# Kernel tuning notes

Measured on AMD Instinct MI355X. Metric: run time of the kernel, lower is better.

The kernel has to match this reference:

```python
import jax, jax.numpy as jnp
import numpy as np


def setup_inputs() -> dict:
    key = jax.random.key(0)
    k1, k2, k3, k4 = jax.random.split(key, 4)
    N, C_in, C_out, H, W, K = 32, 128, 256, 56, 56, 3
    x = jax.random.normal(k1, (N, C_in, H, W), dtype=jnp.float32)
    # ternary weights in {-1, 0, +1}, stored as int8 like the torch buffer
    w_q = jax.random.randint(k2, (C_out, C_in, K, K), -1, 2).astype(jnp.int8)
    s = jax.random.uniform(k3, (C_out, 1, 1), dtype=jnp.float32) + 0.5
    bias = jax.random.normal(k4, (C_out,), dtype=jnp.float32)
    return {"x": x, "w_q": w_q, "s": s, "bias": bias}


def reference(x, w_q, s, bias):
    # y = conv2d(x, w_q.float()) * s + bias, stride=1, padding=1, dilation=1, groups=1
    w = w_q.astype(x.dtype)  # ternary {-1,0,+1} cast to float, as in torch
    y = jax.lax.conv_general_dilated(
        x, w,
        window_strides=(1, 1),
        padding=((1, 1), (1, 1)),
        lhs_dilation=(1, 1),
        rhs_dilation=(1, 1),
        dimension_numbers=("NCHW", "OIHW", "NCHW"),
        feature_group_count=1,
    )
    y = y * s  # s: [C_out,1,1] broadcasts over [N,C_out,H,W]
    y = y + bias.reshape(1, -1, 1, 1)
    return y
```

## Files before the change

kernel.cpp:

```cpp
#include <hip/hip_runtime.h>
#include <hip/hip_bf16.h>

typedef unsigned short ushort_t;

#define N_IMG 32
#define C_IN  128
#define C_OUT 256
#define H_SZ  56
#define W_SZ  56
#define HW_SZ (H_SZ * W_SZ)
#define K_TOT (C_IN * 9)
#define SP_TOT (N_IMG * HW_SZ)

typedef __attribute__((ext_vector_type(8))) short bf16x8;
typedef __attribute__((ext_vector_type(4))) float floatx4;

__device__ __forceinline__ void gl_lds16(const ushort_t* g, ushort_t* l) {
  __builtin_amdgcn_global_load_lds(
      (const __attribute__((address_space(1))) void*)g,
      (__attribute__((address_space(3))) void*)l, 16, 0, 0);
}

__device__ __forceinline__ ushort_t f2bf(float f) {
  __hip_bfloat16 b = __float2bfloat16(f);
  return *reinterpret_cast<ushort_t*>(&b);
}

__global__ void wtrans_kernel(const int* __restrict__ wq, ushort_t* __restrict__ wt,
                              ushort_t* __restrict__ zeros) {
  int tid = threadIdx.x;
  if (blockIdx.x == 0 && tid < 128) zeros[tid] = 0;
  int idx = blockIdx.x * 256 + tid;
  if (idx >= C_OUT * K_TOT) return;
  int co = idx / K_TOT;
  int k  = idx - co * K_TOT;
  int tap = k >> 7;
  int c   = k & 127;
  int kh = tap / 3, kw = tap - kh * 3;
  int v = wq[((co * C_IN + c) * 3 + kh) * 3 + kw];
  wt[idx] = f2bf((float)v);
}

__global__ void xtrans_kernel(const float* __restrict__ x, ushort_t* __restrict__ xt) {
  __shared__ float tile[C_IN * W_SZ];
  int b = blockIdx.x;
  int n = b / H_SZ, h = b - n * H_SZ;
  int tid = threadIdx.x;
  const float* xbase = x + (size_t)n * C_IN * HW_SZ + h * W_SZ;
  for (int idx = tid; idx < C_IN * W_SZ; idx += 256) {
    int c = idx / W_SZ, w = idx - c * W_SZ;
    tile[idx] = xbase[(size_t)c * HW_SZ + w];
  }
  __syncthreads();
  ushort_t* obase = xt + (size_t)b * W_SZ * C_IN;
  for (int idx = tid; idx < W_SZ * (C_IN / 2); idx += 256) {
    int w  = idx >> 6;
    int ci = (idx & 63) * 2;
    unsigned int p = (unsigned int)f2bf(tile[ci * W_SZ + w]) |
                     ((unsigned int)f2bf(tile[(ci + 1) * W_SZ + w]) << 16);
    *(unsigned int*)&obase[(size_t)w * C_IN + ci] = p;
  }
}

__global__ __launch_bounds__(256) void bitconv_kernel(
    const ushort_t* __restrict__ wt, const ushort_t* __restrict__ xt,
    const ushort_t* __restrict__ zeros,
    const float* __restrict__ s, const float* __restrict__ bias,
    float* __restrict__ out) {
  __shared__ ushort_t As[128 * 32];
  __shared__ ushort_t Bs[128 * 32];

  int bid = blockIdx.x;
  int co0 = (bid & 1) * 128;
  int sp0 = (bid >> 1) * 128;

  int tid  = threadIdx.x;
  int lane = tid & 63;
  int wid  = tid >> 6;
  int l15  = lane & 15;
  int quad = lane >> 4;
  int lrow = lane >> 2;
  int lk8  = (lane & 3) * 8;
  int wave_m = (wid >> 1) * 64;
  int wave_n = (wid & 1) * 64;

  const ushort_t* a_src[2];
  ushort_t* a_dst[2];
#pragma unroll
  for (int i = 0; i < 2; ++i) {
    int arow = wid * 32 + i * 16 + lrow;
    a_src[i] = wt + (size_t)(co0 + arow) * K_TOT + lk8;
    a_dst[i] = &As[(wid * 32 + i * 16) * 32];
  }

  int bh[2], bw[2];
  const ushort_t* b_img[2];
  ushort_t* b_dst[2];
#pragma unroll
  for (int i = 0; i < 2; ++i) {
    int sp   = sp0 + wid * 32 + i * 16 + lrow;
    int nimg = sp / HW_SZ;
    int rem  = sp - nimg * HW_SZ;
    bh[i] = rem / W_SZ;
    bw[i] = rem - bh[i] * W_SZ;
    b_img[i] = xt + (size_t)nimg * HW_SZ * C_IN;
    b_dst[i] = &Bs[(wid * 32 + i * 16) * 32];
  }

  floatx4 acc[4][4];
#pragma unroll
  for (int mi = 0; mi < 4; ++mi)
#pragma unroll
    for (int ni = 0; ni < 4; ++ni)
      acc[mi][ni] = (floatx4){0.f, 0.f, 0.f, 0.f};

  for (int tap = 0; tap < 9; ++tap) {
    int dh = tap / 3 - 1;
    int dw = tap - (dh + 1) * 3 - 1;
    const ushort_t* bsrc[2];
#pragma unroll
    for (int i = 0; i < 2; ++i) {
      int hh2 = bh[i] + dh, ww2 = bw[i] + dw;
      bool valid = (hh2 >= 0) & (hh2 < H_SZ) & (ww2 >= 0) & (ww2 < W_SZ);
      bsrc[i] = valid ? (b_img[i] + (size_t)(hh2 * W_SZ + ww2) * C_IN + lk8)
                      : (zeros + lk8);
    }
    int ktap = tap * C_IN;
#pragma unroll
    for (int c0 = 0; c0 < C_IN; c0 += 32) {
#pragma unroll
      for (int i = 0; i < 2; ++i) {
        gl_lds16(a_src[i] + ktap + c0, a_dst[i]);
        gl_lds16(bsrc[i] + c0, b_dst[i]);
      }
      __syncthreads();
      bf16x8 af[4], bfv[4];
#pragma unroll
      for (int mi = 0; mi < 4; ++mi)
        af[mi] = *(const bf16x8*)&As[(wave_m + mi * 16 + l15) * 32 + quad * 8];
#pragma unroll
      for (int ni = 0; ni < 4; ++ni)
        bfv[ni] = *(const bf16x8*)&Bs[(wave_n + ni * 16 + l15) * 32 + quad * 8];
#pragma unroll
      for (int mi = 0; mi < 4; ++mi)
#pragma unroll
        for (int ni = 0; ni < 4; ++ni)
          acc[mi][ni] = __builtin_amdgcn_mfma_f32_16x16x32_bf16(
              af[mi], bfv[ni], acc[mi][ni], 0, 0, 0);
      __syncthreads();
    }
  }

  int spl_[4], nimg_[4];
#pragma unroll
  for (int ni = 0; ni < 4; ++ni) {
    int sp = sp0 + wave_n + ni * 16 + l15;
    int nimg = sp / HW_SZ;
    nimg_[ni] = nimg;
    spl_[ni]  = sp - nimg * HW_SZ;
  }
#pragma unroll
  for (int mi = 0; mi < 4; ++mi) {
#pragma unroll
    for (int r = 0; r < 4; ++r) {
      int co = co0 + wave_m + mi * 16 + quad * 4 + r;
      float sv = s[co];
      float bv = bias[co];
#pragma unroll
      for (int ni = 0; ni < 4; ++ni) {
        out[((size_t)nimg_[ni] * C_OUT + co) * HW_SZ + spl_[ni]] =
            acc[mi][ni][r] * sv + bv;
      }
    }
  }
}

extern "C" void kernel_launch(void* const* d_in, const int* in_sizes, int n_in,
                              void* d_out, int out_size, void* d_ws, size_t ws_size,
                              hipStream_t stream) {
  const float* x    = (const float*)d_in[0];
  const int*   wq   = (const int*)d_in[1];
  const float* s    = (const float*)d_in[2];
  const float* bias = (const float*)d_in[3];
  float* out = (float*)d_out;

  char* ws = (char*)d_ws;
  ushort_t* zeros = (ushort_t*)ws;
  ushort_t* wt    = (ushort_t*)(ws + 256);
  ushort_t* xt    = (ushort_t*)(ws + 590080);

  hipLaunchKernelGGL(wtrans_kernel, dim3((C_OUT * K_TOT) / 256), dim3(256), 0, stream,
                     wq, wt, zeros);
  hipLaunchKernelGGL(xtrans_kernel, dim3(N_IMG * H_SZ), dim3(256), 0, stream, x, xt);
  hipLaunchKernelGGL(bitconv_kernel, dim3((C_OUT / 128) * (SP_TOT / 128)), dim3(256),
                     0, stream, wt, xt, zeros, s, bias, out);
}
```

Measured before the change: 250.5 us.

## Double K-tile depth, swizzle block order, and retile input transpose kernel

The conv GEMM main loop now stages 64 channels per LDS tile instead of 32 and issues two MFMA k-substeps per barrier pair. This halves the number of __syncthreads rounds, at the cost of doubling LDS use. Block indices are remapped so that pairs of co-tiles for nearby spatial tiles run adjacently, which is meant to improve L2 reuse of the input. The NCHW-to-NHWC bf16 transpose kernel now uses 64x64 tiles with float4 loads and a padded LDS stride, to cut bank conflicts and improve coalescing.

```diff
diff --git a/kernel.cpp b/kernel.cpp
--- a/kernel.cpp
+++ b/kernel.cpp
@@ -41,24 +41,37 @@
   wt[idx] = f2bf((float)v);
 }
 
-__global__ void xtrans_kernel(const float* __restrict__ x, ushort_t* __restrict__ xt) {
-  __shared__ float tile[C_IN * W_SZ];
+#define LDT 69
+__global__ __launch_bounds__(256) void xtrans_kernel(const float* __restrict__ x,
+                                                     ushort_t* __restrict__ xt) {
+  __shared__ float tile[64 * LDT];
   int b = blockIdx.x;
-  int n = b / H_SZ, h = b - n * H_SZ;
-  int tid = threadIdx.x;
-  const float* xbase = x + (size_t)n * C_IN * HW_SZ + h * W_SZ;
-  for (int idx = tid; idx < C_IN * W_SZ; idx += 256) {
-    int c = idx / W_SZ, w = idx - c * W_SZ;
-    tile[idx] = xbase[(size_t)c * HW_SZ + w];
+  int n = b / 98;
+  int r = b - n * 98;
+  int cg = r / 49;
+  int hwg = r - cg * 49;
+  int hw0 = hwg * 64, c0 = cg * 64;
+  int t = threadIdx.x;
+  int cl = t >> 4;
+  int f4 = t & 15;
+  const float* xb = x + ((size_t)(n * C_IN + c0) * HW_SZ + hw0);
+#pragma unroll
+  for (int p = 0; p < 4; ++p) {
+    int c = p * 16 + cl;
+    float4 v = *(const float4*)(xb + (size_t)c * HW_SZ + f4 * 4);
+    float* dst = &tile[c * LDT + f4 * 4];
+    dst[0] = v.x; dst[1] = v.y; dst[2] = v.z; dst[3] = v.w;
   }
   __syncthreads();
-  ushort_t* obase = xt + (size_t)b * W_SZ * C_IN;
-  for (int idx = tid; idx < W_SZ * (C_IN / 2); idx += 256) {
-    int w  = idx >> 6;
-    int ci = (idx & 63) * 2;
-    unsigned int p = (unsigned int)f2bf(tile[ci * W_SZ + w]) |
-                     ((unsigned int)f2bf(tile[(ci + 1) * W_SZ + w]) << 16);
-    *(unsigned int*)&obase[(size_t)w * C_IN + ci] = p;
+  int cp  = t & 31;
+  int hwl = t >> 5;
+  ushort_t* ob = xt + (size_t)(n * HW_SZ + hw0) * C_IN + c0;
+#pragma unroll
+  for (int p = 0; p < 8; ++p) {
+    int hw = p * 8 + hwl;
+    unsigned int u = (unsigned int)f2bf(tile[(2 * cp) * LDT + hw]) |
+                     ((unsigned int)f2bf(tile[(2 * cp + 1) * LDT + hw]) << 16);
+    *(unsigned int*)&ob[(size_t)hw * C_IN + 2 * cp] = u;
   }
 }
 
@@ -67,44 +80,35 @@
     const ushort_t* __restrict__ zeros,
     const float* __restrict__ s, const float* __restrict__ bias,
     float* __restrict__ out) {
-  __shared__ ushort_t As[128 * 32];
-  __shared__ ushort_t Bs[128 * 32];
-
-  int bid = blockIdx.x;
-  int co0 = (bid & 1) * 128;
-  int sp0 = (bid >> 1) * 128;
+  __shared__ ushort_t As[128 * 64];
+  __shared__ ushort_t Bs[128 * 64];
+
+  int d = blockIdx.x;
+  int sp_idx = (d >> 4) * 8 + (d & 7);
+  int co0 = ((d >> 3) & 1) * 128;
+  int sp0 = sp_idx * 128;
 
   int tid  = threadIdx.x;
   int lane = tid & 63;
   int wid  = tid >> 6;
   int l15  = lane & 15;
   int quad = lane >> 4;
-  int lrow = lane >> 2;
-  int lk8  = (lane & 3) * 8;
+  int lrow8 = lane >> 3;
+  int lk8   = (lane & 7) * 8;
   int wave_m = (wid >> 1) * 64;
   int wave_n = (wid & 1) * 64;
 
-  const ushort_t* a_src[2];
-  ushort_t* a_dst[2];
-#pragma unroll
-  for (int i = 0; i < 2; ++i) {
-    int arow = wid * 32 + i * 16 + lrow;
-    a_src[i] = wt + (size_t)(co0 + arow) * K_TOT + lk8;
-    a_dst[i] = &As[(wid * 32 + i * 16) * 32];
-  }
-
-  int bh[2], bw[2];
-  const ushort_t* b_img[2];
-  ushort_t* b_dst[2];
-#pragma unroll
-  for (int i = 0; i < 2; ++i) {
-    int sp   = sp0 + wid * 32 + i * 16 + lrow;
+  const ushort_t* a_src0 = wt + (size_t)(co0 + wid * 32 + lrow8) * K_TOT + lk8;
+  int bh[4], bw[4];
+  const ushort_t* b_img[4];
+#pragma unroll
+  for (int j = 0; j < 4; ++j) {
+    int sp   = sp0 + wid * 32 + j * 8 + lrow8;
     int nimg = sp / HW_SZ;
     int rem  = sp - nimg * HW_SZ;
-    bh[i] = rem / W_SZ;
-    bw[i] = rem - bh[i] * W_SZ;
-    b_img[i] = xt + (size_t)nimg * HW_SZ * C_IN;
-    b_dst[i] = &Bs[(wid * 32 + i * 16) * 32];
+    bh[j] = rem / W_SZ;
+    bw[j] = rem - bh[j] * W_SZ;
+    b_img[j] = xt + (size_t)nimg * HW_SZ * C_IN;
   }
 
   floatx4 acc[4][4];
@@ -117,36 +121,42 @@
   for (int tap = 0; tap < 9; ++tap) {
     int dh = tap / 3 - 1;
     int dw = tap - (dh + 1) * 3 - 1;
-    const ushort_t* bsrc[2];
-#pragma unroll
-    for (int i = 0; i < 2; ++i) {
-      int hh2 = bh[i] + dh, ww2 = bw[i] + dw;
+    const ushort_t* bsrc[4];
+#pragma unroll
+    for (int j = 0; j < 4; ++j) {
+      int hh2 = bh[j] + dh, ww2 = bw[j] + dw;
       bool valid = (hh2 >= 0) & (hh2 < H_SZ) & (ww2 >= 0) & (ww2 < W_SZ);
-      bsrc[i] = valid ? (b_img[i] + (size_t)(hh2 * W_SZ + ww2) * C_IN + lk8)
+      bsrc[j] = valid ? (b_img[j] + (size_t)(hh2 * W_SZ + ww2) * C_IN + lk8)
                       : (zeros + lk8);
     }
     int ktap = tap * C_IN;
 #pragma unroll
-    for (int c0 = 0; c0 < C_IN; c0 += 32) {
-#pragma unroll
-      for (int i = 0; i < 2; ++i) {
-        gl_lds16(a_src[i] + ktap + c0, a_dst[i]);
-        gl_lds16(bsrc[i] + c0, b_dst[i]);
+    for (int c0 = 0; c0 < C_IN; c0 += 64) {
+#pragma unroll
+      for (int j = 0; j < 4; ++j) {
+        gl_lds16(a_src0 + (size_t)j * 8 * K_TOT + ktap + c0,
+                 &As[(wid * 32 + j * 8) * 64]);
+        gl_lds16(bsrc[j] + c0, &Bs[(wid * 32 + j * 8) * 64]);
       }
       __syncthreads();
-      bf16x8 af[4], bfv[4];
-#pragma unroll
-      for (int mi = 0; mi < 4; ++mi)
-        af[mi] = *(const bf16x8*)&As[(wave_m + mi * 16 + l15) * 32 + quad * 8];
-#pragma unroll
-      for (int ni = 0; ni < 4; ++ni)
-        bfv[ni] = *(const bf16x8*)&Bs[(wave_n + ni * 16 + l15) * 32 + quad * 8];
-#pragma unroll
-      for (int mi = 0; mi < 4; ++mi)
+#pragma unroll
+      for (int ksub = 0; ksub < 2; ++ksub) {
+        bf16x8 af[4], bfv[4];
+#pragma unroll
+        for (int mi = 0; mi < 4; ++mi)
+          af[mi] = *(const bf16x8*)&As[(wave_m + mi * 16 + l15) * 64 +
+                                       ksub * 32 + quad * 8];
 #pragma unroll
         for (int ni = 0; ni < 4; ++ni)
-          acc[mi][ni] = __builtin_amdgcn_mfma_f32_16x16x32_bf16(
-              af[mi], bfv[ni], acc[mi][ni], 0, 0, 0);
+          bfv[ni] = *(const bf16x8*)&Bs[(wave_n + ni * 16 + l15) * 64 +
+                                        ksub * 32 + quad * 8];
+#pragma unroll
+        for (int mi = 0; mi < 4; ++mi)
+#pragma unroll
+          for (int ni = 0; ni < 4; ++ni)
+            acc[mi][ni] = __builtin_amdgcn_mfma_f32_16x16x32_bf16(
+                af[mi], bfv[ni], acc[mi][ni], 0, 0, 0);
+      }
       __syncthreads();
     }
   }
@@ -191,7 +201,7 @@
 
   hipLaunchKernelGGL(wtrans_kernel, dim3((C_OUT * K_TOT) / 256), dim3(256), 0, stream,
                      wq, wt, zeros);
-  hipLaunchKernelGGL(xtrans_kernel, dim3(N_IMG * H_SZ), dim3(256), 0, stream, x, xt);
+  hipLaunchKernelGGL(xtrans_kernel, dim3(N_IMG * 98), dim3(256), 0, stream, x, xt);
   hipLaunchKernelGGL(bitconv_kernel, dim3((C_OUT / 128) * (SP_TOT / 128)), dim3(256),
                      0, stream, wt, xt, zeros, s, bias, out);
 }
```

New measurement: 239.8 us. -4.3%, faster.

## Pre-pad input to 64-wide rows and tile spatial dimension by image rows

Applied to the files above, without the earlier changes.

Input is transposed into a zero-padded NHWC bf16 buffer with 58 rows of 64 columns, so the conv GEMM loads each tap by a fixed offset with no boundary checks or zero-buffer redirect. Spatial tiles become two padded image rows, with a masked store of the 56 valid columns, and blocks are remapped so consecutive tiles land on the same XCD. This removes per-tap address math and branches but spends about an eighth of the MFMA work on padding columns and writes a larger intermediate.

```diff
diff --git a/kernel.cpp b/kernel.cpp
--- a/kernel.cpp
+++ b/kernel.cpp
@@ -10,7 +10,9 @@
 #define W_SZ  56
 #define HW_SZ (H_SZ * W_SZ)
 #define K_TOT (C_IN * 9)
-#define SP_TOT (N_IMG * HW_SZ)
+#define WP 64
+#define HP 58
+#define ROW_E (WP * C_IN)
 
 typedef __attribute__((ext_vector_type(8))) short bf16x8;
 typedef __attribute__((ext_vector_type(4))) float floatx4;
@@ -26,11 +28,8 @@
   return *reinterpret_cast<ushort_t*>(&b);
 }
 
-__global__ void wtrans_kernel(const int* __restrict__ wq, ushort_t* __restrict__ wt,
-                              ushort_t* __restrict__ zeros) {
-  int tid = threadIdx.x;
-  if (blockIdx.x == 0 && tid < 128) zeros[tid] = 0;
-  int idx = blockIdx.x * 256 + tid;
+__global__ void wtrans_kernel(const int* __restrict__ wq, ushort_t* __restrict__ wt) {
+  int idx = blockIdx.x * 256 + threadIdx.x;
   if (idx >= C_OUT * K_TOT) return;
   int co = idx / K_TOT;
   int k  = idx - co * K_TOT;
@@ -41,70 +40,85 @@
   wt[idx] = f2bf((float)v);
 }
 
-__global__ void xtrans_kernel(const float* __restrict__ x, ushort_t* __restrict__ xt) {
-  __shared__ float tile[C_IN * W_SZ];
+__global__ __launch_bounds__(256) void xpad_kernel(const float* __restrict__ x,
+                                                   ushort_t* __restrict__ xp) {
   int b = blockIdx.x;
-  int n = b / H_SZ, h = b - n * H_SZ;
-  int tid = threadIdx.x;
-  const float* xbase = x + (size_t)n * C_IN * HW_SZ + h * W_SZ;
-  for (int idx = tid; idx < C_IN * W_SZ; idx += 256) {
-    int c = idx / W_SZ, w = idx - c * W_SZ;
-    tile[idx] = xbase[(size_t)c * HW_SZ + w];
+  int t = threadIdx.x;
+  ushort_t* row = xp + (size_t)b * ROW_E;
+  int n = b / HP;
+  int h1 = b - n * HP;
+  if (b >= N_IMG * HP || h1 == 0 || h1 == HP - 1) {
+    uint4 z = {0u, 0u, 0u, 0u};
+    uint4* r4 = (uint4*)row;
+#pragma unroll
+    for (int i = 0; i < 4; ++i) r4[i * 256 + t] = z;
+    return;
+  }
+  __shared__ float tile[C_IN * 57];
+  int h = h1 - 1;
+  const float* xb = x + (size_t)n * C_IN * HW_SZ + h * W_SZ;
+#pragma unroll
+  for (int i = 0; i < 7; ++i) {
+    int idx = i * 256 + t;
+    int c = idx / 14, f = idx - c * 14;
+    float4 v = *(const float4*)(xb + (size_t)c * HW_SZ + f * 4);
+    float* dst = &tile[c * 57 + f * 4];
+    dst[0] = v.x; dst[1] = v.y; dst[2] = v.z; dst[3] = v.w;
   }
   __syncthreads();
-  ushort_t* obase = xt + (size_t)b * W_SZ * C_IN;
-  for (int idx = tid; idx < W_SZ * (C_IN / 2); idx += 256) {
-    int w  = idx >> 6;
-    int ci = (idx & 63) * 2;
-    unsigned int p = (unsigned int)f2bf(tile[ci * W_SZ + w]) |
-                     ((unsigned int)f2bf(tile[(ci + 1) * W_SZ + w]) << 16);
-    *(unsigned int*)&obase[(size_t)w * C_IN + ci] = p;
+  unsigned int* r32 = (unsigned int*)row;
+#pragma unroll
+  for (int i = 0; i < 16; ++i) {
+    int idx = i * 256 + t;
+    int wp = idx >> 6, cp = idx & 63;
+    unsigned int u = 0;
+    if (wp >= 1 && wp <= W_SZ) {
+      int w = wp - 1;
+      u = (unsigned int)f2bf(tile[(2 * cp) * 57 + w]) |
+          ((unsigned int)f2bf(tile[(2 * cp + 1) * 57 + w]) << 16);
+    }
+    r32[wp * 64 + cp] = u;
   }
 }
 
 __global__ __launch_bounds__(256) void bitconv_kernel(
-    const ushort_t* __restrict__ wt, const ushort_t* __restrict__ xt,
-    const ushort_t* __restrict__ zeros,
+    const ushort_t* __restrict__ wt, const ushort_t* __restrict__ xp,
     const float* __restrict__ s, const float* __restrict__ bias,
     float* __restrict__ out) {
   __shared__ ushort_t As[128 * 32];
   __shared__ ushort_t Bs[128 * 32];
 
-  int bid = blockIdx.x;
-  int co0 = (bid & 1) * 128;
-  int sp0 = (bid >> 1) * 128;
+  int d = blockIdx.x;
+  int xcd = d & 7;
+  int r   = d >> 3;
+  int co0 = (r & 1) * 128;
+  int sp_tile = xcd * 112 + (r >> 1);
+  int nh0 = sp_tile * 2;
+  int n  = nh0 / H_SZ;
+  int hh = nh0 - n * H_SZ;
 
   int tid  = threadIdx.x;
   int lane = tid & 63;
   int wid  = tid >> 6;
   int l15  = lane & 15;
   int quad = lane >> 4;
-  int lrow = lane >> 2;
-  int lk8  = (lane & 3) * 8;
   int wave_m = (wid >> 1) * 64;
   int wave_n = (wid & 1) * 64;
+  int lrow = lane >> 2;
+  int lchk = (lane & 3) * 8;
 
   const ushort_t* a_src[2];
+  const ushort_t* b_src[2];
   ushort_t* a_dst[2];
-#pragma unroll
-  for (int i = 0; i < 2; ++i) {
-    int arow = wid * 32 + i * 16 + lrow;
-    a_src[i] = wt + (size_t)(co0 + arow) * K_TOT + lk8;
-    a_dst[i] = &As[(wid * 32 + i * 16) * 32];
-  }
-
-  int bh[2], bw[2];
-  const ushort_t* b_img[2];
   ushort_t* b_dst[2];
 #pragma unroll
-  for (int i = 0; i < 2; ++i) {
-    int sp   = sp0 + wid * 32 + i * 16 + lrow;
-    int nimg = sp / HW_SZ;
-    int rem  = sp - nimg * HW_SZ;
-    bh[i] = rem / W_SZ;
-    bw[i] = rem - bh[i] * W_SZ;
-    b_img[i] = xt + (size_t)nimg * HW_SZ * C_IN;
-    b_dst[i] = &Bs[(wid * 32 + i * 16) * 32];
+  for (int g = 0; g < 2; ++g) {
+    int rrow = wid * 32 + g * 16 + lrow;
+    a_src[g] = wt + (size_t)(co0 + rrow) * K_TOT + lchk;
+    int hrow = rrow >> 6, wpp = (rrow & 63) + 1;
+    b_src[g] = xp + (size_t)((n * HP + hh + 1 + hrow) * WP + wpp) * C_IN + lchk;
+    a_dst[g] = &As[(wid * 32 + g * 16) * 32];
+    b_dst[g] = &Bs[(wid * 32 + g * 16) * 32];
   }
 
   floatx4 acc[4][4];
@@ -117,21 +131,14 @@
   for (int tap = 0; tap < 9; ++tap) {
     int dh = tap / 3 - 1;
     int dw = tap - (dh + 1) * 3 - 1;
-    const ushort_t* bsrc[2];
-#pragma unroll
-    for (int i = 0; i < 2; ++i) {
-      int hh2 = bh[i] + dh, ww2 = bw[i] + dw;
-      bool valid = (hh2 >= 0) & (hh2 < H_SZ) & (ww2 >= 0) & (ww2 < W_SZ);
-      bsrc[i] = valid ? (b_img[i] + (size_t)(hh2 * W_SZ + ww2) * C_IN + lk8)
-                      : (zeros + lk8);
-    }
-    int ktap = tap * C_IN;
+    int boff = dh * (WP * C_IN) + dw * C_IN;
+    int aoff = tap * C_IN;
 #pragma unroll
     for (int c0 = 0; c0 < C_IN; c0 += 32) {
 #pragma unroll
-      for (int i = 0; i < 2; ++i) {
-        gl_lds16(a_src[i] + ktap + c0, a_dst[i]);
-        gl_lds16(bsrc[i] + c0, b_dst[i]);
+      for (int g = 0; g < 2; ++g) {
+        gl_lds16(a_src[g] + aoff + c0, a_dst[g]);
+        gl_lds16(b_src[g] + boff + c0, b_dst[g]);
       }
       __syncthreads();
       bf16x8 af[4], bfv[4];
@@ -151,25 +158,20 @@
     }
   }
 
-  int spl_[4], nimg_[4];
-#pragma unroll
-  for (int ni = 0; ni < 4; ++ni) {
-    int sp = sp0 + wave_n + ni * 16 + l15;
-    int nimg = sp / HW_SZ;
-    nimg_[ni] = nimg;
-    spl_[ni]  = sp - nimg * HW_SZ;
-  }
+  int h_out = hh + (wid & 1);
 #pragma unroll
   for (int mi = 0; mi < 4; ++mi) {
 #pragma unroll
-    for (int r = 0; r < 4; ++r) {
-      int co = co0 + wave_m + mi * 16 + quad * 4 + r;
+    for (int rg = 0; rg < 4; ++rg) {
+      int co = co0 + wave_m + mi * 16 + quad * 4 + rg;
       float sv = s[co];
       float bv = bias[co];
+      float* ob = out + (size_t)(n * C_OUT + co) * HW_SZ + h_out * W_SZ;
 #pragma unroll
       for (int ni = 0; ni < 4; ++ni) {
-        out[((size_t)nimg_[ni] * C_OUT + co) * HW_SZ + spl_[ni]] =
-            acc[mi][ni][r] * sv + bv;
+        int wpp = ni * 16 + l15;
+        if (wpp < W_SZ)
+          ob[wpp] = acc[mi][ni][rg] * sv + bv;
       }
     }
   }
@@ -185,13 +187,12 @@
   float* out = (float*)d_out;
 
   char* ws = (char*)d_ws;
-  ushort_t* zeros = (ushort_t*)ws;
-  ushort_t* wt    = (ushort_t*)(ws + 256);
-  ushort_t* xt    = (ushort_t*)(ws + 590080);
+  ushort_t* wt = (ushort_t*)ws;
+  ushort_t* xp = (ushort_t*)(ws + 589824);
 
   hipLaunchKernelGGL(wtrans_kernel, dim3((C_OUT * K_TOT) / 256), dim3(256), 0, stream,
-                     wq, wt, zeros);
-  hipLaunchKernelGGL(xtrans_kernel, dim3(N_IMG * H_SZ), dim3(256), 0, stream, x, xt);
-  hipLaunchKernelGGL(bitconv_kernel, dim3((C_OUT / 128) * (SP_TOT / 128)), dim3(256),
-                     0, stream, wt, xt, zeros, s, bias, out);
+                     wq, wt);
+  hipLaunchKernelGGL(xpad_kernel, dim3(N_IMG * HP + 1), dim3(256), 0, stream, x, xp);
+  hipLaunchKernelGGL(bitconv_kernel, dim3(1792), dim3(256), 0, stream,
+                     wt, xp, s, bias, out);
 }
```

Result: faster. 228.2 us (-8.9%).
